# Performance work log

Measured on AMD Instinct MI355X. Metric: run time of the kernel, lower is better.

## Reference

```python
import jax, jax.numpy as jnp
import numpy as np

B, T, E, H, VF, C = 4, 8192, 512, 8, 2, 256
KD = E // H          # key dim per head = 64
HD = E * VF // H     # value head dim = 128


def _rel_pos():
    decay = np.log(1.0 - 2.0 ** (-5.0 - np.arange(H, dtype=np.float64)))  # [H]
    ang = 1.0 / (10000 ** np.linspace(0, 1, KD // 2))
    ang = np.repeat(ang, 2)                                  # [KD]
    idx = np.arange(T)
    sin = np.sin(idx[:, None] * ang[None, :]).astype(np.float32)
    cos = np.cos(idx[:, None] * ang[None, :]).astype(np.float32)
    bi = np.arange(C)
    diff = bi[:, None] - bi[None, :]
    m = np.where(diff >= 0, np.exp(decay[:, None, None] * diff), 0.0)  # [H,C,C]
    last = m[:, -1]                                          # [H,C]
    vid = (last / last.sum(-1, keepdims=True))[:, :, None]   # [H,C,1]
    scale = np.sqrt(m.sum(-1, keepdims=True))                # [H,C,1]
    mask = (m / scale).astype(np.float32)
    cross_decay = np.exp(decay * C)[:, None, None].astype(np.float32)  # [H,1,1]
    qid = np.exp(decay[:, None] * (bi + 1))[:, :, None]      # [H,C,1]
    qid = (qid / (scale / last.sum(-1)[:, None, None])).astype(np.float32)
    return sin, cos, mask, cross_decay, qid, vid.astype(np.float32)


def setup_inputs() -> dict:
    key = jax.random.key(0)
    ks = jax.random.split(key, 6)
    sin, cos, mask, cross_decay, qid, vid = _rel_pos()
    s = 0.02
    return {
        'x': jax.random.normal(ks[0], (B, T, E), jnp.float32),
        'sin': jnp.asarray(sin), 'cos': jnp.asarray(cos),
        'mask': jnp.asarray(mask), 'cross_decay': jnp.asarray(cross_decay),
        'query_inner_decay': jnp.asarray(qid), 'value_inner_decay': jnp.asarray(vid),
        'Wq': jax.random.normal(ks[1], (E, E), jnp.float32) * s,
        'Wk': jax.random.normal(ks[2], (E, E), jnp.float32) * s,
        'Wv': jax.random.normal(ks[3], (E, E * VF), jnp.float32) * s,
        'Wg': jax.random.normal(ks[4], (E, E * VF), jnp.float32) * s,
        'Wo': jax.random.normal(ks[5], (E * VF, E), jnp.float32) * s,
    }


def _rotate_every_two(x):
    x1, x2 = x[..., ::2], x[..., 1::2]
    return jnp.stack((-x2, x1), axis=-1).reshape(x.shape)


def _theta_shift(x, sin, cos):
    return x * cos + _rotate_every_two(x) * sin


def reference(x, sin, cos, mask, cross_decay, query_inner_decay, value_inner_decay, Wq, Wk, Wv, Wg, Wo):
    Bz, Tl, _ = x.shape
    q = (x @ Wq).reshape(Bz, Tl, H, KD).transpose(0, 2, 1, 3)               # [B,H,T,KD]
    k = ((x @ Wk) * (KD ** -0.5)).reshape(Bz, Tl, H, KD).transpose(0, 2, 1, 3)
    v = x @ Wv                                                              # [B,T,E*VF]
    g = x @ Wg
    qr = _theta_shift(q, sin, cos)
    kr = _theta_shift(k, sin, cos)

    NC = Tl // C
    qr = qr.reshape(Bz, H, NC, C, KD).transpose(0, 2, 1, 3, 4)              # [B,NC,H,C,KD]
    kr = kr.reshape(Bz, H, NC, C, KD).transpose(0, 2, 1, 3, 4)
    vc = v.reshape(Bz, NC, C, H, HD).transpose(0, 1, 3, 2, 4)               # [B,NC,H,C,HD]

    qk = jnp.einsum('bnhck,bnhdk->bnhcd', qr, kr) * mask                    # decay-masked intra-chunk
    inner_scale = jnp.clip(jax.lax.stop_gradient(jnp.abs(qk)).sum(-1, keepdims=True), 1.0, None)
    qk = qk / inner_scale
    inner_output = jnp.einsum('bnhcd,bnhde->bnhce', qk, vc)                 # [B,NC,H,C,HD]

    kv = jnp.einsum('bnhck,bnhcd->bnhkd', kr, vc * value_inner_decay)       # [B,NC,H,KD,HD]

    def step(carry, kv_i):
        kv_state, kv_scale = carry
        out = (kv_state / kv_scale, kv_scale)
        kv_state = kv_state * cross_decay + kv_i
        kv_scale = jnp.clip(
            jax.lax.stop_gradient(jnp.abs(kv_state)).sum(-2, keepdims=True).max(-1, keepdims=True),
            1.0, None)
        return (kv_state, kv_scale), out

    kv_state0 = jnp.zeros((Bz, H, KD, HD), x.dtype)
    kv_scale0 = jnp.ones((Bz, H, 1, 1), x.dtype)
    _, (kv_recurrent, cross_scale) = jax.lax.scan(step, (kv_state0, kv_scale0), jnp.swapaxes(kv, 0, 1))
    kv_recurrent = jnp.swapaxes(kv_recurrent, 0, 1)                         # [B,NC,H,KD,HD]
    cross_scale = jnp.swapaxes(cross_scale, 0, 1)                           # [B,NC,H,1,1]

    all_scale = jnp.maximum(inner_scale, cross_scale)
    cross_output = jnp.einsum('bnhck,bnhkd->bnhcd', qr * query_inner_decay, kv_recurrent)
    output = inner_output / (all_scale / inner_scale) + cross_output / (all_scale / cross_scale)
    output = output.transpose(0, 1, 3, 2, 4)                                # [B,NC,C,H,HD]
    # group_norm: RMSNorm over head_dim, no affine
    output = output * jax.lax.rsqrt(jnp.mean(output ** 2, -1, keepdims=True) + 1e-6)
    output = output.reshape(Bz, Tl, H * HD)
    output = jax.nn.silu(g) * output
    return output @ Wo
```

## Files before the change

### kernel.cpp

```cpp
#include <hip/hip_runtime.h>
#include <cmath>

#define Bz 4
#define Tt 8192
#define Ee 512
#define Hh 8
#define Cc 256
#define KD 64
#define HD 128
#define NC 32
#define EV 1024
#define Mrows (Bz*Tt)

typedef unsigned short u16;
typedef __attribute__((ext_vector_type(4))) float f32x4;
typedef __attribute__((ext_vector_type(8))) short s16x8;

__device__ __forceinline__ u16 f2b(float f) {
    union { float f; unsigned u; } v; v.f = f;
    unsigned r = v.u + 0x7FFFu + ((v.u >> 16) & 1u);
    return (u16)(r >> 16);
}
__device__ __forceinline__ float b2f(u16 u) {
    union { unsigned u; float f; } v; v.u = ((unsigned)u) << 16;
    return v.f;
}
#define MFMA16(a, b, c) __builtin_amdgcn_mfma_f32_16x16x32_bf16((a), (b), (c), 0, 0, 0)

__device__ __forceinline__ void glds16(const u16* g, u16* l) {
    __builtin_amdgcn_global_load_lds(
        (const __attribute__((address_space(1))) unsigned int*)g,
        (__attribute__((address_space(3))) unsigned int*)l,
        16, 0, 0);
}

__device__ __forceinline__ size_t fpk(int row, int k, int K) {
    return (size_t)(row >> 4) * (K * 16) + (k >> 5) * 512 + ((k >> 3) & 3) * 128 +
           (row & 15) * 8 + (k & 7);
}

__global__ __launch_bounds__(256) void cast_x_k(const float* __restrict__ x,
                                                u16* __restrict__ xb) {
    size_t i = ((size_t)blockIdx.x * 256 + threadIdx.x) * 4;
    float4 v = *(const float4*)(x + i);
    int m = (int)(i >> 9), e = (int)(i & 511);
    ushort4 o;
    o.x = f2b(v.x); o.y = f2b(v.y); o.z = f2b(v.z); o.w = f2b(v.w);
    *(ushort4*)(xb + fpk(m, e, 512)) = o;
}

__global__ __launch_bounds__(256) void castT_k(const float* __restrict__ W,
                                               u16* __restrict__ Wt,
                                               int K, int N, float scale) {
    __shared__ float tile[32][33];
    int k0 = blockIdx.y * 32, n0 = blockIdx.x * 32;
    int r = threadIdx.x >> 3, c4 = (threadIdx.x & 7) * 4;
    float4 v = *(const float4*)(W + (size_t)(k0 + r) * N + n0 + c4);
    tile[r][c4] = v.x; tile[r][c4 + 1] = v.y; tile[r][c4 + 2] = v.z; tile[r][c4 + 3] = v.w;
    __syncthreads();
    ushort4 o;
    o.x = f2b(tile[c4 + 0][r] * scale);
    o.y = f2b(tile[c4 + 1][r] * scale);
    o.z = f2b(tile[c4 + 2][r] * scale);
    o.w = f2b(tile[c4 + 3][r] * scale);
    *(ushort4*)(Wt + fpk(n0 + r, k0 + c4, K)) = o;
}

template <int EPI>
__global__ __launch_bounds__(256) void gemm_mfma(const u16* __restrict__ A,
                                                 const u16* __restrict__ Bt,
                                                 void* __restrict__ Cout,
                                                 int K, int N,
                                                 const float* __restrict__ sn,
                                                 const float* __restrict__ cs) {
    __shared__ __align__(16) u16 pool[20480];
    u16 (*lds)[8192] = (u16(*)[8192])pool;
    int tid = threadIdx.x;
    int lane = tid & 63, wid = tid >> 6;
    int cL = lane & 15, quad = lane >> 4;
    int M0 = blockIdx.y * 8, N0 = blockIdx.x * 8;
    int m0 = blockIdx.y * 128 + (wid & 1) * 64;
    int n0 = blockIdx.x * 128 + (wid >> 1) * 64;
    const int KT = K * 16;
    const int NK = K >> 5;

#define STAGE(buf, kc) do {                                                        \
        size_t kofs = (size_t)(kc) * 512 + lane * 8;                               \
        glds16(A  + (size_t)(M0 + wid * 2    ) * KT + kofs,                        \
               &lds[buf][(wid * 2    ) * 512]);                                    \
        glds16(A  + (size_t)(M0 + wid * 2 + 1) * KT + kofs,                        \
               &lds[buf][(wid * 2 + 1) * 512]);                                    \
        glds16(Bt + (size_t)(N0 + wid * 2    ) * KT + kofs,                        \
               &lds[buf][4096 + (wid * 2    ) * 512]);                             \
        glds16(Bt + (size_t)(N0 + wid * 2 + 1) * KT + kofs,                        \
               &lds[buf][4096 + (wid * 2 + 1) * 512]);                             \
    } while (0)

    STAGE(0, 0);
    __syncthreads();

    f32x4 acc[4][4] = {};
    int mh = (wid & 1) * 4, nh = (wid >> 1) * 4;
    for (int kc = 0; kc < NK; ++kc) {
        int cur = kc & 1;
        if (kc + 1 < NK) STAGE(cur ^ 1, kc + 1);
        s16x8 af[4], bfr[4];
        int fo = quad * 128 + cL * 8;
        #pragma unroll
        for (int mt = 0; mt < 4; ++mt)
            af[mt] = *(const s16x8*)(&lds[cur][(mh + mt) * 512 + fo]);
        #pragma unroll
        for (int nt = 0; nt < 4; ++nt)
            bfr[nt] = *(const s16x8*)(&lds[cur][4096 + (nh + nt) * 512 + fo]);
        #pragma unroll
        for (int mt = 0; mt < 4; ++mt)
            #pragma unroll
            for (int nt = 0; nt < 4; ++nt)
                acc[mt][nt] = MFMA16(af[mt], bfr[nt], acc[mt][nt]);
        __syncthreads();
    }
#undef STAGE
    u16* ep = pool + wid * 5120;

    if (EPI == 0) {
        u16* dst = (u16*)Cout;
        int b = m0 >> 13, h = n0 >> 6, tb = m0 & 8191;
        #pragma unroll
        for (int mt = 0; mt < 4; ++mt)
            #pragma unroll
            for (int nt = 0; nt < 4; ++nt)
                #pragma unroll
                for (int i = 0; i < 4; ++i) {
                    int mrow = mt * 16 + quad * 4 + i;
                    int n = n0 + nt * 16 + cL;
                    float v = acc[mt][nt][i];
                    float p = __shfl_xor(v, 1, 64);
                    int t = tb + mrow, kd = n & 63;
                    float c1 = cs[t * 64 + kd], s1 = sn[t * 64 + kd];
                    float o = (n & 1) ? (v * c1 + p * s1) : (v * c1 - p * s1);
                    ep[mrow * 80 + nt * 16 + cL] = f2b(o);
                }
        u16* dstbh = dst + (size_t)(b * 8 + h) * 524288;
        #pragma unroll
        for (int g2 = 0; g2 < 4; ++g2)
            #pragma unroll
            for (int pass = 0; pass < 2; ++pass) {
                int kcol = pass * 32 + quad * 8;
                s16x8 vv = *(const s16x8*)(ep + (g2 * 16 + cL) * 80 + kcol);
                *(s16x8*)(dstbh + fpk(tb + g2 * 16 + cL, kcol, 64)) = vv;
            }
    } else if (EPI == 1) {
        u16* vt = (u16*)Cout;
        #pragma unroll
        for (int mt = 0; mt < 4; ++mt)
            #pragma unroll
            for (int nt = 0; nt < 4; ++nt) {
                int m = m0 + mt * 16 + quad * 4;
                int n = n0 + nt * 16 + cL;
                int b = m >> 13, t = m & 8191;
                int nn = t >> 8, ccc = t & 255;
                int h = n >> 7, e = n & 127;
                ushort4 pk;
                pk.x = f2b(acc[mt][nt][0]);
                pk.y = f2b(acc[mt][nt][1]);
                pk.z = f2b(acc[mt][nt][2]);
                pk.w = f2b(acc[mt][nt][3]);
                *(ushort4*)(vt + (((size_t)((b * 8 + h) * 32 + nn)) << 15) +
                            fpk(e, ccc, 256)) = pk;
            }
    } else if (EPI == 2) {
        u16* dst = (u16*)Cout;
        #pragma unroll
        for (int mt = 0; mt < 4; ++mt)
            #pragma unroll
            for (int nt = 0; nt < 4; ++nt)
                #pragma unroll
                for (int i = 0; i < 4; ++i)
                    ep[(mt * 16 + quad * 4 + i) * 80 + nt * 16 + cL] =
                        f2b(acc[mt][nt][i]);
        #pragma unroll
        for (int g2 = 0; g2 < 4; ++g2)
            #pragma unroll
            for (int pass = 0; pass < 2; ++pass) {
                int ncol = pass * 32 + quad * 8;
                s16x8 vv = *(const s16x8*)(ep + (g2 * 16 + cL) * 80 + ncol);
                *(s16x8*)(dst + fpk(m0 + g2 * 16 + cL, n0 + ncol, N)) = vv;
            }
    } else {
        float* dst = (float*)Cout;
        #pragma unroll
        for (int mt = 0; mt < 4; ++mt)
            #pragma unroll
            for (int nt = 0; nt < 4; ++nt)
                #pragma unroll
                for (int i = 0; i < 4; ++i)
                    dst[(size_t)(m0 + mt * 16 + quad * 4 + i) * N + n0 + nt * 16 + cL] =
                        acc[mt][nt][i];
    }
}

__global__ __launch_bounds__(256) void attn_mfma(const u16* __restrict__ qr,
                                                 const u16* __restrict__ kr,
                                                 const u16* __restrict__ vt,
                                                 const float* __restrict__ mask,
                                                 u16* __restrict__ ATT,
                                                 float* __restrict__ iscale_g) {
    __shared__ __align__(16) u16 Ss[64][264];
    __shared__ float partial[4][64];
    __shared__ float sInvL[64];
    int p = blockIdx.x;
    int g = (p & 7) | ((p >> 5) << 3);
    int rtile = (p >> 3) & 3;
    int h = g & 7; int n = (g >> 3) & 31; int b = g >> 8;
    int tid = threadIdx.x, lane = tid & 63, w = tid >> 6;
    int cL = lane & 15, quad = lane >> 4;

    size_t qf_bh = (size_t)(b * 8 + h) * 524288;
    f32x4 acc[4][4] = {};
    if (w <= rtile) {
        const u16* Qb = qr + qf_bh + (size_t)(n * 16 + rtile * 4) * 1024;
        const u16* Kb = kr + qf_bh + (size_t)(n * 16 + w * 4) * 1024;
        #pragma unroll
        for (int kt = 0; kt < 2; ++kt) {
            s16x8 af[4], bfr[4];
            size_t ko = (size_t)kt * 512 + quad * 128 + cL * 8;
            #pragma unroll
            for (int mt = 0; mt < 4; ++mt)
                af[mt] = *(const s16x8*)(Qb + (size_t)mt * 1024 + ko);
            #pragma unroll
            for (int nt = 0; nt < 4; ++nt)
                bfr[nt] = *(const s16x8*)(Kb + (size_t)nt * 1024 + ko);
            #pragma unroll
            for (int mt = 0; mt < 4; ++mt)
                #pragma unroll
                for (int nt = 0; nt < 4; ++nt)
                    acc[mt][nt] = MFMA16(af[mt], bfr[nt], acc[mt][nt]);
        }
    }
    float rs[4][4] = {};
    if (w <= rtile) {
        const float* mb = mask + ((size_t)h << 16);
        #pragma unroll
        for (int mt = 0; mt < 4; ++mt)
            #pragma unroll
            for (int nt = 0; nt < 4; ++nt)
                #pragma unroll
                for (int i = 0; i < 4; ++i) {
                    int r = rtile * 64 + mt * 16 + quad * 4 + i;
                    int d = w * 64 + nt * 16 + cL;
                    float s = acc[mt][nt][i] * mb[r * 256 + d];
                    Ss[mt * 16 + quad * 4 + i][w * 64 + nt * 16 + cL] = f2b(s);
                    rs[mt][i] += fabsf(s);
                }
    }
    #pragma unroll
    for (int mt = 0; mt < 4; ++mt)
        #pragma unroll
        for (int i = 0; i < 4; ++i) {
            float v = rs[mt][i];
            v += __shfl_xor(v, 1, 16);
            v += __shfl_xor(v, 2, 16);
            v += __shfl_xor(v, 4, 16);
            v += __shfl_xor(v, 8, 16);
            if (cL == 0) partial[w][mt * 16 + quad * 4 + i] = v;
        }
    __syncthreads();
    if (tid < 64) {
        float tot = partial[0][tid] + partial[1][tid] + partial[2][tid] + partial[3][tid];
        tot = fmaxf(tot, 1.f);
        iscale_g[((size_t)((b * 32 + n) * 8 + h)) * 256 + rtile * 64 + tid] = tot;
        sInvL[tid] = 1.f / tot;
    }
    __syncthreads();

    f32x4 o[8] = {};
    const u16* Vb = vt + (((size_t)((b * 8 + h) * 32 + n)) << 15);
    int kmax = 2 * (rtile + 1);
    for (int kt = 0; kt < kmax; ++kt) {
        s16x8 a = *(const s16x8*)(&Ss[w * 16 + cL][kt * 32 + quad * 8]);
        #pragma unroll
        for (int nt = 0; nt < 8; ++nt) {
            s16x8 bv = *(const s16x8*)(Vb + (size_t)nt * 4096 + kt * 512 +
                                       quad * 128 + cL * 8);
            o[nt] = MFMA16(a, bv, o[nt]);
        }
    }
    #pragma unroll
    for (int nt = 0; nt < 8; ++nt)
        #pragma unroll
        for (int i = 0; i < 4; ++i) {
            int r = quad * 4 + i;
            Ss[w * 16 + r][nt * 16 + cL] = f2b(o[nt][i] * sInvL[w * 16 + r]);
        }
    size_t obase = ((size_t)b * 8192 + n * 256 + rtile * 64) * 1024 + h * 128;
    #pragma unroll
    for (int pass = 0; pass < 4; ++pass) {
        int e = pass * 32 + quad * 8;
        s16x8 vv = *(const s16x8*)(&Ss[w * 16 + cL][e]);
        *(s16x8*)(ATT + obase + (size_t)(w * 16 + cL) * 1024 + e) = vv;
    }
}

__global__ __launch_bounds__(256) void chunkkv_mfma(const u16* __restrict__ kr,
                                                    const u16* __restrict__ vt,
                                                    const float* __restrict__ vid,
                                                    float* __restrict__ kvT) {
    __shared__ u16 KtL[64][264];
    int bid = blockIdx.x;
    int h = bid & 7; bid >>= 3;
    int n = bid & 31; int b = bid >> 5;
    int tid = threadIdx.x, lane = tid & 63, w = tid >> 6;
    int cL = lane & 15, quad = lane >> 4;
    size_t qf_bh = (size_t)(b * 8 + h) * 524288;
    {
        int c = tid;
        const u16* rp = kr + qf_bh + (size_t)(n * 16 + (c >> 4)) * 1024 + (c & 15) * 8;
        #pragma unroll
        for (int u = 0; u < 8; ++u) {
            s16x8 vv = *(const s16x8*)(rp + (u >> 2) * 512 + (u & 3) * 128);
            #pragma unroll
            for (int j = 0; j < 8; ++j) KtL[u * 8 + j][c] = (u16)vv[j];
        }
    }
    __syncthreads();
    const u16* Vb = vt + (((size_t)((b * 8 + h) * 32 + n)) << 15);
    f32x4 acc[2][4] = {};
    for (int kt = 0; kt < 8; ++kt) {
        float vidv[8];
        #pragma unroll
        for (int j = 0; j < 8; ++j) vidv[j] = vid[h * 256 + kt * 32 + quad * 8 + j];
        s16x8 af[2];
        #pragma unroll
        for (int mt = 0; mt < 2; ++mt) {
            s16x8 raw = *(const s16x8*)(Vb + (size_t)(w * 2 + mt) * 4096 +
                                        kt * 512 + quad * 128 + cL * 8);
            #pragma unroll
            for (int j = 0; j < 8; ++j)
                af[mt][j] = (short)f2b(b2f((u16)raw[j]) * vidv[j]);
        }
        #pragma unroll
        for (int nt = 0; nt < 4; ++nt) {
            s16x8 bv = *(const s16x8*)(&KtL[nt * 16 + cL][kt * 32 + quad * 8]);
            #pragma unroll
            for (int mt = 0; mt < 2; ++mt) acc[mt][nt] = MFMA16(af[mt], bv, acc[mt][nt]);
        }
    }
    float* out = kvT + ((size_t)((b * 32 + n) * 8 + h)) * 8192;
    #pragma unroll
    for (int mt = 0; mt < 2; ++mt)
        #pragma unroll
        for (int nt = 0; nt < 4; ++nt)
            #pragma unroll
            for (int i = 0; i < 4; ++i)
                out[(w * 32 + mt * 16 + quad * 4 + i) * 64 + nt * 16 + cL] = acc[mt][nt][i];
}

__global__ __launch_bounds__(256) void scan_par(const float* __restrict__ kvT,
                                                u16* __restrict__ kvrecb,
                                                const float* __restrict__ cdv,
                                                float* __restrict__ cscale) {
    int bid = blockIdx.x;
    int n = bid & 31; bid >>= 5;
    int h = bid & 7; int b = bid >> 3;
    int tid = threadIdx.x, lane = tid & 63, g = tid >> 6;
    float cd = cdv[h];
    float st[32];
    #pragma unroll
    for (int i = 0; i < 32; ++i) st[i] = 0.f;
    for (int j = 0; j < n; ++j) {
        size_t base = ((size_t)((b * 32 + j) * 8 + h)) * 8192;
        #pragma unroll
        for (int i = 0; i < 32; ++i) {
            int e = g + 4 * i;
            st[i] = st[i] * cd + kvT[base + e * 64 + lane];
        }
    }
    __shared__ float esum[128];
    __shared__ float sSc;
    #pragma unroll
    for (int i = 0; i < 32; ++i) {
        float s = fabsf(st[i]);
        s += __shfl_xor(s, 1, 64);
        s += __shfl_xor(s, 2, 64);
        s += __shfl_xor(s, 4, 64);
        s += __shfl_xor(s, 8, 64);
        s += __shfl_xor(s, 16, 64);
        s += __shfl_xor(s, 32, 64);
        if (lane == 0) esum[g + 4 * i] = s;
    }
    __syncthreads();
    if (tid < 64) {
        float m1 = fmaxf(esum[tid], esum[tid + 64]);
        m1 = fmaxf(m1, __shfl_xor(m1, 1, 64));
        m1 = fmaxf(m1, __shfl_xor(m1, 2, 64));
        m1 = fmaxf(m1, __shfl_xor(m1, 4, 64));
        m1 = fmaxf(m1, __shfl_xor(m1, 8, 64));
        m1 = fmaxf(m1, __shfl_xor(m1, 16, 64));
        m1 = fmaxf(m1, __shfl_xor(m1, 32, 64));
        if (tid == 0) sSc = fmaxf(m1, 1.f);
    }
    __syncthreads();
    float scale = sSc;
    float inv = 1.f / scale;
    size_t baseN = ((size_t)((b * 32 + n) * 8 + h)) * 8192;
    #pragma unroll
    for (int i = 0; i < 32; ++i) {
        int e = g + 4 * i;
        kvrecb[baseN + ((size_t)(lane >> 3) * 128 + e) * 8 + (lane & 7)] = f2b(st[i] * inv);
    }
    if (tid == 0) cscale[(b * 32 + n) * 8 + h] = scale;
}

__global__ __launch_bounds__(256) void cross_mfma(const u16* __restrict__ qr,
                                                  const u16* __restrict__ kvrecb,
                                                  const float* __restrict__ iscale_g,
                                                  const float* __restrict__ cscale_g,
                                                  const float* __restrict__ qid,
                                                  u16* __restrict__ ATT) {
    __shared__ __align__(16) u16 X[4][4608];
    int bid = blockIdx.x;
    int h = bid & 7; bid >>= 3;
    int n = bid & 31; int b = bid >> 5;
    int tid = threadIdx.x, lane = tid & 63, w = tid >> 6;
    int cL = lane & 15, quad = lane >> 4;
    size_t qf_bh = (size_t)(b * 8 + h) * 524288;
    const u16* Qb = qr + qf_bh + (size_t)(n * 16 + w * 4) * 1024;
    const u16* KVb = kvrecb + ((size_t)((b * 32 + n) * 8 + h)) * 8192;
    s16x8 af[4][2];
    #pragma unroll
    for (int mt = 0; mt < 4; ++mt)
        #pragma unroll
        for (int kt = 0; kt < 2; ++kt)
            af[mt][kt] = *(const s16x8*)(Qb + (size_t)mt * 1024 + kt * 512 +
                                         quad * 128 + cL * 8);
    float csc = cscale_g[(b * 32 + n) * 8 + h];
    size_t ibase = ((size_t)((b * 32 + n) * 8 + h)) * 256 + w * 64;
    size_t obase = ((size_t)(b * 8192 + n * 256 + w * 64)) * 1024 + h * 128;
    #pragma unroll
    for (int hn = 0; hn < 2; ++hn) {
        f32x4 acc[4][4] = {};
        #pragma unroll
        for (int kt = 0; kt < 2; ++kt)
            #pragma unroll
            for (int nt = 0; nt < 4; ++nt) {
                int e = (hn * 4 + nt) * 16 + cL;
                s16x8 bv = *(const s16x8*)(KVb + ((size_t)(kt * 4 + quad) * 128 + e) * 8);
                #pragma unroll
                for (int mt = 0; mt < 4; ++mt)
                    acc[mt][nt] = MFMA16(af[mt][kt], bv, acc[mt][nt]);
            }
        #pragma unroll
        for (int mt = 0; mt < 4; ++mt)
            #pragma unroll
            for (int i = 0; i < 4; ++i) {
                int r = mt * 16 + quad * 4 + i;
                float isc = iscale_g[ibase + r];
                float alls = fmaxf(isc, csc);
                float fC = (csc / alls) * qid[h * 256 + w * 64 + r];
                #pragma unroll
                for (int nt = 0; nt < 4; ++nt)
                    X[w][r * 72 + nt * 16 + cL] = f2b(acc[mt][nt][i] * fC);
            }
        #pragma unroll
        for (int g2 = 0; g2 < 4; ++g2)
            #pragma unroll
            for (int pass = 0; pass < 2; ++pass) {
                int r2 = g2 * 16 + cL;
                float isc2 = iscale_g[ibase + r2];
                float fI2 = isc2 / fmaxf(isc2, csc);
                int e = pass * 32 + quad * 8;
                s16x8 sv = *(const s16x8*)(&X[w][r2 * 72 + e]);
                size_t oi = obase + (size_t)r2 * 1024 + hn * 64 + e;
                s16x8 pv = *(const s16x8*)(ATT + oi);
                s16x8 ov;
                #pragma unroll
                for (int j = 0; j < 8; ++j)
                    ov[j] = (short)f2b(b2f((u16)pv[j]) * fI2 + b2f((u16)sv[j]));
                *(s16x8*)(ATT + oi) = ov;
            }
    }
}

__global__ __launch_bounds__(256) void rms_silu(const u16* __restrict__ ATT,
                                                u16* __restrict__ g) {
    __shared__ u16 att_s[16 * 1036];
    __shared__ float rmsv[16][8];
    int tile = blockIdx.x;
    int tid = threadIdx.x;
    size_t abase = (size_t)tile * 16 * 1024;
    int head = tid >> 5;
    #pragma unroll
    for (int jj = 0; jj < 16; ++jj) {
        ushort4 v = *(const ushort4*)(ATT + abase + (size_t)jj * 1024 + tid * 4);
        *(ushort4*)(att_s + jj * 1036 + tid * 4) = v;
        float x0 = b2f(v.x), x1 = b2f(v.y), x2 = b2f(v.z), x3 = b2f(v.w);
        float ss = x0 * x0 + x1 * x1 + x2 * x2 + x3 * x3;
        ss += __shfl_xor(ss, 1, 32);
        ss += __shfl_xor(ss, 2, 32);
        ss += __shfl_xor(ss, 4, 32);
        ss += __shfl_xor(ss, 8, 32);
        ss += __shfl_xor(ss, 16, 32);
        if ((tid & 31) == 0)
            rmsv[jj][head] = rsqrtf(ss * (1.f / 128.f) + 1e-6f);
    }
    __syncthreads();
    size_t gbase = (size_t)tile * 16384;
    #pragma unroll
    for (int it = 0; it < 16; ++it) {
        int p = it * 1024 + tid * 4;
        int e = ((p >> 9) << 5) | (((p >> 7) & 3) << 3) | (p & 7);
        int r = (p >> 3) & 15;
        ushort4 gv = *(const ushort4*)(g + gbase + p);
        ushort4 av = *(const ushort4*)(att_s + r * 1036 + e);
        float rms = rmsv[r][e >> 7];
        float x0 = b2f(av.x), x1 = b2f(av.y), x2 = b2f(av.z), x3 = b2f(av.w);
        float g0 = b2f(gv.x), g1 = b2f(gv.y), g2 = b2f(gv.z), g3 = b2f(gv.w);
        ushort4 ov;
        ov.x = f2b((g0 / (1.f + __expf(-g0))) * x0 * rms);
        ov.y = f2b((g1 / (1.f + __expf(-g1))) * x1 * rms);
        ov.z = f2b((g2 / (1.f + __expf(-g2))) * x2 * rms);
        ov.w = f2b((g3 / (1.f + __expf(-g3))) * x3 * rms);
        *(ushort4*)(g + gbase + p) = ov;
    }
}

extern "C" void kernel_launch(void* const* d_in, const int* in_sizes, int n_in,
                              void* d_out, int out_size, void* d_ws, size_t ws_size,
                              hipStream_t stream) {
    const float* x    = (const float*)d_in[0];
    const float* sn   = (const float*)d_in[1];
    const float* cs   = (const float*)d_in[2];
    const float* mask = (const float*)d_in[3];
    const float* cdv  = (const float*)d_in[4];
    const float* qid  = (const float*)d_in[5];
    const float* vid  = (const float*)d_in[6];
    const float* Wq   = (const float*)d_in[7];
    const float* Wk   = (const float*)d_in[8];
    const float* Wv   = (const float*)d_in[9];
    const float* Wg   = (const float*)d_in[10];
    const float* Wo   = (const float*)d_in[11];
    float* out = (float*)d_out;

    char* w = (char*)d_ws;
    u16* qr     = (u16*)w;   w += (size_t)16777216 * 2;
    u16* kr     = (u16*)w;   w += (size_t)16777216 * 2;
    u16* vt     = (u16*)w;   w += (size_t)33554432 * 2;
    u16* xbf    = (u16*)w;   w += (size_t)16777216 * 2;
    u16* wqT    = (u16*)w;   w += (size_t)262144 * 2;
    u16* wkT    = (u16*)w;   w += (size_t)262144 * 2;
    u16* wvT    = (u16*)w;   w += (size_t)524288 * 2;
    u16* wgT    = (u16*)w;   w += (size_t)524288 * 2;
    u16* woT    = (u16*)w;   w += (size_t)524288 * 2;
    float* kvT  = (float*)w; w += (size_t)8388608 * 4;
    u16* kvrecb = (u16*)w;   w += (size_t)8388608 * 2;
    float* iscale = (float*)w; w += (size_t)262144 * 4;
    float* cscale = (float*)w; w += (size_t)1024 * 4;

    u16* gbuf = qr;
    u16* ATT  = (u16*)d_out;

    dim3 blk(256);
    cast_x_k<<<dim3(16384), blk, 0, stream>>>(x, xbf);
    castT_k<<<dim3(16, 16), blk, 0, stream>>>(Wq, wqT, 512, 512, 1.0f);
    castT_k<<<dim3(16, 16), blk, 0, stream>>>(Wk, wkT, 512, 512, 0.125f);
    castT_k<<<dim3(32, 16), blk, 0, stream>>>(Wv, wvT, 512, 1024, 1.0f);
    castT_k<<<dim3(32, 16), blk, 0, stream>>>(Wg, wgT, 512, 1024, 1.0f);
    castT_k<<<dim3(16, 32), blk, 0, stream>>>(Wo, woT, 1024, 512, 1.0f);
    gemm_mfma<0><<<dim3(4, 256), blk, 0, stream>>>(xbf, wqT, qr, 512, 512, sn, cs);
    gemm_mfma<0><<<dim3(4, 256), blk, 0, stream>>>(xbf, wkT, kr, 512, 512, sn, cs);
    gemm_mfma<1><<<dim3(8, 256), blk, 0, stream>>>(xbf, wvT, vt, 512, 1024, nullptr, nullptr);
    attn_mfma<<<dim3(4096), blk, 0, stream>>>(qr, kr, vt, mask, ATT, iscale);
    chunkkv_mfma<<<dim3(1024), blk, 0, stream>>>(kr, vt, vid, kvT);
    scan_par<<<dim3(1024), blk, 0, stream>>>(kvT, kvrecb, cdv, cscale);
    cross_mfma<<<dim3(1024), blk, 0, stream>>>(qr, kvrecb, iscale, cscale, qid, ATT);
    gemm_mfma<2><<<dim3(8, 256), blk, 0, stream>>>(xbf, wgT, gbuf, 512, 1024, nullptr, nullptr);
    rms_silu<<<dim3(2048), blk, 0, stream>>>(ATT, gbuf);
    gemm_mfma<3><<<dim3(4, 256), blk, 0, stream>>>(gbuf, woT, out, 1024, 512, nullptr, nullptr);
}
```

Measured before the change: 647.3 us.

## Cast decay mask to bf16, prefetch scan chunks, use HIP bf16 conversion

Adds a kernel that converts the fp32 decay mask to bf16 once, so the attention kernel reads half the mask bytes in its scaling loop. The prefix scan over chunk KV states now software-pipelines its loads, fetching chunk j+1 into registers while accumulating chunk j. The manual float-to-bf16 rounding is replaced by the HIP intrinsic. The cost is an extra small launch, bf16 precision loss in the mask values, and higher register pressure in the scan kernel.

```diff
diff --git a/kernel.cpp b/kernel.cpp
--- a/kernel.cpp
+++ b/kernel.cpp
@@ -1,4 +1,5 @@
 #include <hip/hip_runtime.h>
+#include <hip/hip_bf16.h>
 #include <cmath>
 
 #define Bz 4
@@ -17,9 +18,8 @@
 typedef __attribute__((ext_vector_type(8))) short s16x8;
 
 __device__ __forceinline__ u16 f2b(float f) {
-    union { float f; unsigned u; } v; v.f = f;
-    unsigned r = v.u + 0x7FFFu + ((v.u >> 16) & 1u);
-    return (u16)(r >> 16);
+    __hip_bfloat16 h = __float2bfloat16(f);
+    return *reinterpret_cast<u16*>(&h);
 }
 __device__ __forceinline__ float b2f(u16 u) {
     union { unsigned u; float f; } v; v.u = ((unsigned)u) << 16;
@@ -47,6 +47,15 @@
     ushort4 o;
     o.x = f2b(v.x); o.y = f2b(v.y); o.z = f2b(v.z); o.w = f2b(v.w);
     *(ushort4*)(xb + fpk(m, e, 512)) = o;
+}
+
+__global__ __launch_bounds__(256) void cast_mask_k(const float* __restrict__ m,
+                                                   u16* __restrict__ mb) {
+    size_t i = ((size_t)blockIdx.x * 256 + threadIdx.x) * 4;
+    float4 v = *(const float4*)(m + i);
+    ushort4 o;
+    o.x = f2b(v.x); o.y = f2b(v.y); o.z = f2b(v.z); o.w = f2b(v.w);
+    *(ushort4*)(mb + i) = o;
 }
 
 __global__ __launch_bounds__(256) void castT_k(const float* __restrict__ W,
@@ -202,7 +211,7 @@
 __global__ __launch_bounds__(256) void attn_mfma(const u16* __restrict__ qr,
                                                  const u16* __restrict__ kr,
                                                  const u16* __restrict__ vt,
-                                                 const float* __restrict__ mask,
+                                                 const u16* __restrict__ maskb,
                                                  u16* __restrict__ ATT,
                                                  float* __restrict__ iscale_g) {
     __shared__ __align__(16) u16 Ss[64][264];
@@ -239,7 +248,7 @@
     }
     float rs[4][4] = {};
     if (w <= rtile) {
-        const float* mb = mask + ((size_t)h << 16);
+        const u16* mb = maskb + ((size_t)h << 16);
         #pragma unroll
         for (int mt = 0; mt < 4; ++mt)
             #pragma unroll
@@ -248,7 +257,7 @@
                 for (int i = 0; i < 4; ++i) {
                     int r = rtile * 64 + mt * 16 + quad * 4 + i;
                     int d = w * 64 + nt * 16 + cL;
-                    float s = acc[mt][nt][i] * mb[r * 256 + d];
+                    float s = acc[mt][nt][i] * b2f(mb[r * 256 + d]);
                     Ss[mt * 16 + quad * 4 + i][w * 64 + nt * 16 + cL] = f2b(s);
                     rs[mt][i] += fabsf(s);
                 }
@@ -364,16 +373,24 @@
     int h = bid & 7; int b = bid >> 3;
     int tid = threadIdx.x, lane = tid & 63, g = tid >> 6;
     float cd = cdv[h];
-    float st[32];
-    #pragma unroll
-    for (int i = 0; i < 32; ++i) st[i] = 0.f;
+    float st[32], cur[32], nxt[32];
+    #pragma unroll
+    for (int i = 0; i < 32; ++i) { st[i] = 0.f; nxt[i] = 0.f; }
+    if (n > 0) {
+        size_t base0 = ((size_t)((b * 32) * 8 + h)) * 8192;
+        #pragma unroll
+        for (int i = 0; i < 32; ++i) cur[i] = kvT[base0 + (g + 4 * i) * 64 + lane];
+    }
     for (int j = 0; j < n; ++j) {
-        size_t base = ((size_t)((b * 32 + j) * 8 + h)) * 8192;
-        #pragma unroll
-        for (int i = 0; i < 32; ++i) {
-            int e = g + 4 * i;
-            st[i] = st[i] * cd + kvT[base + e * 64 + lane];
-        }
+        if (j + 1 < n) {
+            size_t basen = ((size_t)((b * 32 + j + 1) * 8 + h)) * 8192;
+            #pragma unroll
+            for (int i = 0; i < 32; ++i) nxt[i] = kvT[basen + (g + 4 * i) * 64 + lane];
+        }
+        #pragma unroll
+        for (int i = 0; i < 32; ++i) st[i] = st[i] * cd + cur[i];
+        #pragma unroll
+        for (int i = 0; i < 32; ++i) cur[i] = nxt[i];
     }
     __shared__ float esum[128];
     __shared__ float sSc;
@@ -555,12 +572,14 @@
     u16* kvrecb = (u16*)w;   w += (size_t)8388608 * 2;
     float* iscale = (float*)w; w += (size_t)262144 * 4;
     float* cscale = (float*)w; w += (size_t)1024 * 4;
+    u16* maskb  = (u16*)w;   w += (size_t)524288 * 2;
 
     u16* gbuf = qr;
     u16* ATT  = (u16*)d_out;
 
     dim3 blk(256);
     cast_x_k<<<dim3(16384), blk, 0, stream>>>(x, xbf);
+    cast_mask_k<<<dim3(512), blk, 0, stream>>>(mask, maskb);
     castT_k<<<dim3(16, 16), blk, 0, stream>>>(Wq, wqT, 512, 512, 1.0f);
     castT_k<<<dim3(16, 16), blk, 0, stream>>>(Wk, wkT, 512, 512, 0.125f);
     castT_k<<<dim3(32, 16), blk, 0, stream>>>(Wv, wvT, 512, 1024, 1.0f);
@@ -569,7 +588,7 @@
     gemm_mfma<0><<<dim3(4, 256), blk, 0, stream>>>(xbf, wqT, qr, 512, 512, sn, cs);
     gemm_mfma<0><<<dim3(4, 256), blk, 0, stream>>>(xbf, wkT, kr, 512, 512, sn, cs);
     gemm_mfma<1><<<dim3(8, 256), blk, 0, stream>>>(xbf, wvT, vt, 512, 1024, nullptr, nullptr);
-    attn_mfma<<<dim3(4096), blk, 0, stream>>>(qr, kr, vt, mask, ATT, iscale);
+    attn_mfma<<<dim3(4096), blk, 0, stream>>>(qr, kr, vt, maskb, ATT, iscale);
     chunkkv_mfma<<<dim3(1024), blk, 0, stream>>>(kr, vt, vid, kvT);
     scan_par<<<dim3(1024), blk, 0, stream>>>(kvT, kvrecb, cdv, cscale);
     cross_mfma<<<dim3(1024), blk, 0, stream>>>(qr, kvrecb, iscale, cscale, qid, ATT);
```

New measurement: 642.7 us. Within noise of the previous version (-0.7%).
